# Kernel tuning notes

Measured on AMD Instinct MI355X. Metric: run time of the kernel, lower is better.

## Reference

```python
import jax, jax.numpy as jnp
import numpy as np


def lstm_dir(x, w_ih, w_hh, b, reverse):
    # x: [N, L, E]; torch gate order i, f, g, o; b = b_ih + b_hh combined
    if reverse:
        x = x[:, ::-1, :]
    H = w_hh.shape[1]
    N = x.shape[0]
    xg = jnp.einsum('nle,ge->nlg', x, w_ih) + b  # [N, L, 4H]
    def step(carry, xt):
        h, c = carry
        g = xt + h @ w_hh.T
        i, f, gg, o = jnp.split(g, 4, axis=-1)
        c = jax.nn.sigmoid(f) * c + jax.nn.sigmoid(i) * jnp.tanh(gg)
        h = jax.nn.sigmoid(o) * jnp.tanh(c)
        return (h, c), h
    init = (jnp.zeros((N, H), x.dtype), jnp.zeros((N, H), x.dtype))
    _, hs = jax.lax.scan(step, init, jnp.swapaxes(xg, 0, 1))
    hs = jnp.swapaxes(hs, 0, 1)  # [N, L, H]
    if reverse:
        hs = hs[:, ::-1, :]
    return hs


def setup_inputs() -> dict:
    key = jax.random.key(0)
    ks = jax.random.split(key, 10)
    B, D, S, V, E, H = 32, 32, 64, 32000, 256, 512
    tok = jax.random.randint(ks[0], (B, D, S), 1, V)
    slen = jax.random.randint(ks[1], (B, D), 8, S + 1)  # ragged sentence lengths
    docs = jnp.where(jnp.arange(S)[None, None, :] < slen[..., None], tok, 0)
    doc_lens = jax.random.randint(ks[2], (B,), 1, D + 1)  # ragged doc lengths
    embed_weight = jax.random.normal(ks[3], (V, E), jnp.float32) * 0.02
    def p(k, shp):
        return jax.random.normal(k, shp, jnp.float32) * 0.05
    return dict(
        docs=docs, doc_lens=doc_lens, max_doc_len=D,
        embed_weight=embed_weight,
        w_ih_f=p(ks[4], (4 * H, E)), w_hh_f=p(ks[5], (4 * H, H)), b_f=p(ks[6], (4 * H,)),
        w_ih_b=p(ks[7], (4 * H, E)), w_hh_b=p(ks[8], (4 * H, H)), b_b=p(ks[9], (4 * H,)),
    )


def reference(docs, doc_lens, max_doc_len, embed_weight, w_ih_f, w_hh_f, b_f, w_ih_b, w_hh_b, b_b):
    B, D, S = docs.shape
    sents = docs.reshape(B * D, S)                     # all sentences, incl. invalid slots
    sent_lens = jnp.sum(jnp.sign(sents), axis=1)       # nonzero-token count per sentence
    x = embed_weight[sents]                            # [BD, S, E]
    out_f = lstm_dir(x, w_ih_f, w_hh_f, b_f, False)
    out_b = lstm_dir(x, w_ih_b, w_hh_b, b_b, True)
    out = jnp.concatenate([out_f, out_b], axis=-1)     # [BD, S, 2H]
    # avg_pool1d over first sent_lens timesteps (segment mean)
    tmask = (jnp.arange(S)[None, :] < sent_lens[:, None]).astype(out.dtype)
    denom = jnp.maximum(sent_lens, 1).astype(out.dtype)
    pooled = jnp.sum(out * tmask[:, :, None], axis=1) / denom[:, None]  # [BD, 2H]
    pooled = pooled.reshape(B, D, -1)
    # pad_doc: zero out sentence slots beyond each doc_len (scatter-pad)
    dmask = jnp.arange(D)[None, :] < doc_lens[:, None]
    return jnp.where(dmask[:, :, None], pooled, jnp.zeros((), pooled.dtype))
```

## Files before the change

kernel.cpp:

```cpp
#include <hip/hip_runtime.h>
#include <hip/hip_bf16.h>
#include <hip/hip_cooperative_groups.h>

namespace cg = cooperative_groups;

typedef __attribute__((ext_vector_type(4))) float f32x4;
typedef __attribute__((ext_vector_type(8))) short s16x8;

#define SEQ   64
#define EMB   256
#define HID   512
#define NROW  1024
#define NTHR  512
#define NGRID 256
#define LDS_BYTES 98304

#define XB_OFF   0ull
#define WHH_OFF  (XB_OFF + 65536ull * EMB * 2)
#define WIH_OFF  (WHH_OFF + 2ull * 2048 * HID * 2)
#define HB_OFF   (WIH_OFF + 2ull * 2048 * EMB * 2)
#define SL_OFF   (HB_OFF + 4ull * NROW * HID * 2)
#define BAR_OFF  (SL_OFF + 4096ull)
#define XCDW_OFF (BAR_OFF + 64ull)

__device__ __forceinline__ unsigned short f2bf(float f) {
    union { float f; unsigned u; } x; x.f = f;
    unsigned r = x.u + 0x7fffu + ((x.u >> 16) & 1u);
    return (unsigned short)(r >> 16);
}
__device__ __forceinline__ void cvt8(unsigned short* dst, const float* src) {
    f32x4 v0 = *(const f32x4*)src;
    f32x4 v1 = *(const f32x4*)(src + 4);
    s16x8 o;
    o[0] = (short)f2bf(v0[0]); o[1] = (short)f2bf(v0[1]);
    o[2] = (short)f2bf(v0[2]); o[3] = (short)f2bf(v0[3]);
    o[4] = (short)f2bf(v1[0]); o[5] = (short)f2bf(v1[1]);
    o[6] = (short)f2bf(v1[2]); o[7] = (short)f2bf(v1[3]);
    *(s16x8*)dst = o;
}
__device__ __forceinline__ float sigf(float x)  { return 1.0f / (1.0f + __expf(-x)); }
__device__ __forceinline__ float tanh_(float x) { return 2.0f / (1.0f + __expf(-2.0f * x)) - 1.0f; }

__global__ void __launch_bounds__(NTHR, 2)
lstm_enc(const int* __restrict__ docs, const int* __restrict__ doc_lens,
         const float* __restrict__ embed,
         const float* __restrict__ w_ih_f, const float* __restrict__ w_hh_f, const float* __restrict__ b_f,
         const float* __restrict__ w_ih_b, const float* __restrict__ w_hh_b, const float* __restrict__ b_b,
         float* __restrict__ out, unsigned char* __restrict__ ws)
{
    extern __shared__ unsigned short Wf[];

    unsigned short* xb  = (unsigned short*)(ws + XB_OFF);
    unsigned short* whh = (unsigned short*)(ws + WHH_OFF);
    unsigned short* wih = (unsigned short*)(ws + WIH_OFF);
    unsigned short* hb  = (unsigned short*)(ws + HB_OFF);
    int*       sl   = (int*)(ws + SL_OFF);
    unsigned*  bar  = (unsigned*)(ws + BAR_OFF);
    unsigned*  xcdw = (unsigned*)(ws + XCDW_OFF);

    const int tid = threadIdx.x;
    const int bid = blockIdx.x;
    const int gid = bid * NTHR + tid;

    for (int i = 0; i < 16; ++i) {
        int slot = gid + i * (NGRID * NTHR);
        int row = slot >> 5;
        int e   = (slot & 31) << 3;
        int tok = docs[row];
        cvt8(xb + (size_t)slot * 8, embed + (size_t)tok * EMB + e);
    }
    cvt8(whh + (size_t)gid * 8,             w_hh_f + (size_t)gid * 8);
    cvt8(whh + (size_t)(gid + 131072) * 8,  w_hh_b + (size_t)gid * 8);
    {
        int dir0 = gid >> 16;
        int idx  = gid & 65535;
        cvt8(wih + (size_t)gid * 8, (dir0 ? w_ih_b : w_ih_f) + (size_t)idx * 8);
    }
    {
        s16x8 z = {0,0,0,0,0,0,0,0};
        *(s16x8*)(hb + (size_t)gid * 8) = z;
    }
    if (gid < NROW) {
        int c = 0;
        const int* dr = docs + gid * SEQ;
        for (int s2 = 0; s2 < SEQ; ++s2) c += (dr[s2] != 0);
        sl[gid] = c;
    }
    if (gid < 8) bar[gid] = 0u;

    if (tid == 0) {
        unsigned xcd_id;
        asm("s_getreg_b32 %0, hwreg(HW_REG_XCC_ID)" : "=s"(xcd_id));
        __hip_atomic_store(xcdw + bid, xcd_id, __ATOMIC_RELAXED, __HIP_MEMORY_SCOPE_AGENT);
    }

    cg::this_grid().sync();

    const int grp = bid & 7;
    const int dir = grp >> 2;
    const int rg  = grp & 3;
    const int cgd = bid >> 3;
    const int rowbase = rg * 256;
    const int hubase  = cgd * 16;

    bool fast;
    {
        unsigned mine = __hip_atomic_load(xcdw + bid, __ATOMIC_RELAXED, __HIP_MEMORY_SCOPE_AGENT);
        unsigned same = 1u;
        for (int j = 0; j < 32; ++j) {
            unsigned o = __hip_atomic_load(xcdw + (grp + 8 * j), __ATOMIC_RELAXED, __HIP_MEMORY_SCOPE_AGENT);
            same &= (o == mine) ? 1u : 0u;
        }
        fast = (same != 0u);
    }

    {
        const unsigned short* whh_d = whh + (size_t)dir * 2048 * HID;
        const unsigned short* wih_d = wih + (size_t)dir * 2048 * EMB;
        for (int s2 = 0; s2 < 12; ++s2) {
            int S = s2 * NTHR + tid;
            int f = S >> 6, lane_s = S & 63;
            int kc = f >> 2, g = f & 3;
            int l15s = lane_s & 15, lqs = lane_s >> 4;
            int gn = g * HID + hubase + l15s;
            int k  = kc * 32 + lqs * 8;
            const unsigned short* src = (k < HID)
                ? (whh_d + (size_t)gn * HID + k)
                : (wih_d + (size_t)gn * EMB + (k - HID));
            *(s16x8*)(Wf + (size_t)S * 8) = *(const s16x8*)src;
        }
    }
    __syncthreads();

    const int wid = tid >> 6, lane = tid & 63, l15 = lane & 15, lq = lane >> 4;
    const int hu = hubase + l15;
    const float* bsrc = dir ? b_b : b_f;
    const float bi_ = bsrc[hu], bf_ = bsrc[HID + hu], bg_ = bsrc[2 * HID + hu], bo_ = bsrc[3 * HID + hu];

    int rA[2];
    rA[0] = rowbase + wid * 32 + l15;
    rA[1] = rowbase + wid * 32 + 16 + l15;

    int gr8[8]; int sl8[8]; float c8[8], pool8[8];
    #pragma unroll
    for (int rf = 0; rf < 2; ++rf)
        #pragma unroll
        for (int r = 0; r < 4; ++r) {
            int k8 = rf * 4 + r;
            gr8[k8] = rowbase + wid * 32 + rf * 16 + lq * 4 + r;
            sl8[k8] = sl[gr8[k8]];
            c8[k8] = 0.f; pool8[k8] = 0.f;
        }

    #pragma unroll 1
    for (int t = 0; t < SEQ; ++t) {
        const int te = dir ? (SEQ - 1 - t) : t;
        const unsigned short* hrd = hb + (size_t)((t & 1) * 2 + dir) * NROW * HID;
        unsigned short* hwr       = hb + (size_t)((((t + 1) & 1)) * 2 + dir) * NROW * HID;

        f32x4 acc[2][4];
        #pragma unroll
        for (int rf = 0; rf < 2; ++rf)
            #pragma unroll
            for (int g = 0; g < 4; ++g)
                acc[rf][g] = (f32x4){0.f, 0.f, 0.f, 0.f};

        auto ldA = [&](s16x8* dst, int kc) {
            #pragma unroll
            for (int rf = 0; rf < 2; ++rf) {
                const unsigned short* p = (kc < 16)
                    ? hrd + (size_t)rA[rf] * HID + kc * 32 + lq * 8
                    : xb + ((size_t)rA[rf] * SEQ + te) * EMB + (kc - 16) * 32 + lq * 8;
                dst[rf] = *(const s16x8*)p;
            }
        };

        s16x8 Abuf[2][2];
        ldA(Abuf[0], 0);
        #pragma unroll
        for (int kc = 0; kc < 24; ++kc) {
            if (kc < 23) ldA(Abuf[(kc + 1) & 1], kc + 1);
            s16x8 Bf[4];
            #pragma unroll
            for (int g = 0; g < 4; ++g)
                Bf[g] = *(const s16x8*)(Wf + ((size_t)(kc * 4 + g) * 64 + lane) * 8);
            #pragma unroll
            for (int rf = 0; rf < 2; ++rf)
                #pragma unroll
                for (int g = 0; g < 4; ++g)
                    acc[rf][g] = __builtin_amdgcn_mfma_f32_16x16x32_bf16(
                        Abuf[kc & 1][rf], Bf[g], acc[rf][g], 0, 0, 0);
        }

        unsigned short hv8[8];
        #pragma unroll
        for (int rf = 0; rf < 2; ++rf) {
            #pragma unroll
            for (int r = 0; r < 4; ++r) {
                int k8 = rf * 4 + r;
                float iv = acc[rf][0][r] + bi_;
                float fv = acc[rf][1][r] + bf_;
                float gv = acc[rf][2][r] + bg_;
                float ov = acc[rf][3][r] + bo_;
                float cc = sigf(fv) * c8[k8] + sigf(iv) * tanh_(gv);
                c8[k8] = cc;
                float hh = sigf(ov) * tanh_(cc);
                hv8[k8] = f2bf(hh);
                if (te < sl8[k8]) pool8[k8] += hh;
            }
        }
        if (fast) {
            #pragma unroll
            for (int k8 = 0; k8 < 8; ++k8)
                hwr[(size_t)gr8[k8] * HID + hu] = hv8[k8];
        } else {
            #pragma unroll
            for (int k8 = 0; k8 < 8; ++k8)
                __hip_atomic_store(hwr + (size_t)gr8[k8] * HID + hu, hv8[k8],
                                   __ATOMIC_RELAXED, __HIP_MEMORY_SCOPE_AGENT);
        }

        __syncthreads();
        if (tid == 0) {
            __hip_atomic_fetch_add(bar + grp, 1u, __ATOMIC_RELAXED, __HIP_MEMORY_SCOPE_AGENT);
            unsigned tgt = 32u * (unsigned)(t + 1);
            while (__hip_atomic_load(bar + grp, __ATOMIC_RELAXED, __HIP_MEMORY_SCOPE_AGENT) < tgt)
                __builtin_amdgcn_s_sleep(1);
            if (fast) {
                asm volatile("buffer_inv" ::: "memory");
            } else {
                (void)__hip_atomic_load(bar + grp, __ATOMIC_ACQUIRE, __HIP_MEMORY_SCOPE_AGENT);
            }
        }
        __syncthreads();
    }

    #pragma unroll
    for (int k8 = 0; k8 < 8; ++k8) {
        int gr = gr8[k8];
        int b = gr >> 5, d = gr & 31;
        float denom = (float)(sl8[k8] > 0 ? sl8[k8] : 1);
        float v = (d < doc_lens[b]) ? (pool8[k8] / denom) : 0.f;
        out[(size_t)gr * 1024 + (size_t)dir * HID + hu] = v;
    }
}

extern "C" void kernel_launch(void* const* d_in, const int* in_sizes, int n_in,
                              void* d_out, int out_size, void* d_ws, size_t ws_size,
                              hipStream_t stream) {
    const int*   docs     = (const int*)d_in[0];
    const int*   doc_lens = (const int*)d_in[1];
    const float* embed    = (const float*)d_in[3];
    const float* w_ih_f   = (const float*)d_in[4];
    const float* w_hh_f   = (const float*)d_in[5];
    const float* b_f      = (const float*)d_in[6];
    const float* w_ih_b   = (const float*)d_in[7];
    const float* w_hh_b   = (const float*)d_in[8];
    const float* b_b      = (const float*)d_in[9];
    float* out = (float*)d_out;
    unsigned char* wsp = (unsigned char*)d_ws;

    (void)in_sizes; (void)n_in; (void)out_size; (void)ws_size;

    hipFuncSetAttribute((const void*)lstm_enc,
                        hipFuncAttributeMaxDynamicSharedMemorySize, LDS_BYTES);

    void* args[] = { &docs, &doc_lens, &embed, &w_ih_f, &w_hh_f, &b_f,
                     &w_ih_b, &w_hh_b, &b_b, &out, &wsp };
    hipLaunchCooperativeKernel((void*)lstm_enc, dim3(NGRID), dim3(NTHR),
                               args, (unsigned)LDS_BYTES, stream);
}
```

Before: 1.090 ms.

## Overlap next-step input projection with barrier wait and pad barrier counters

Splits the per-step GEMM into an input-projection part (x·W_ih plus bias folded into the accumulator init) and a recurrent part (h·W_hh). After writing h, each block signals arrival and then computes the next timestep's input projection before waiting on the barrier, so that work hides the barrier latency. Barrier counters are also padded to separate cache lines per group to avoid false sharing. The accumulators now stay live across the barrier, which raises register pressure, and the fetch-add stays relaxed before the spin, relying on the existing release and acquire handling.

After: 1.013 ms. -7.1%, faster.

```diff
diff --git a/kernel.cpp b/kernel.cpp
--- a/kernel.cpp
+++ b/kernel.cpp
@@ -14,6 +14,7 @@
 #define NTHR  512
 #define NGRID 256
 #define LDS_BYTES 98304
+#define BSTRIDE 32
 
 #define XB_OFF   0ull
 #define WHH_OFF  (XB_OFF + 65536ull * EMB * 2)
@@ -21,7 +22,7 @@
 #define HB_OFF   (WIH_OFF + 2ull * 2048 * EMB * 2)
 #define SL_OFF   (HB_OFF + 4ull * NROW * HID * 2)
 #define BAR_OFF  (SL_OFF + 4096ull)
-#define XCDW_OFF (BAR_OFF + 64ull)
+#define XCDW_OFF (BAR_OFF + 8ull * BSTRIDE * 4ull)
 
 __device__ __forceinline__ unsigned short f2bf(float f) {
     union { float f; unsigned u; } x; x.f = f;
@@ -86,7 +87,7 @@
         for (int s2 = 0; s2 < SEQ; ++s2) c += (dr[s2] != 0);
         sl[gid] = c;
     }
-    if (gid < 8) bar[gid] = 0u;
+    if (gid < 8 * BSTRIDE) bar[gid] = 0u;
 
     if (tid == 0) {
         unsigned xcd_id;
@@ -102,6 +103,7 @@
     const int cgd = bid >> 3;
     const int rowbase = rg * 256;
     const int hubase  = cgd * 16;
+    unsigned* mybar = bar + grp * BSTRIDE;
 
     bool fast;
     {
@@ -135,7 +137,9 @@
     const int wid = tid >> 6, lane = tid & 63, l15 = lane & 15, lq = lane >> 4;
     const int hu = hubase + l15;
     const float* bsrc = dir ? b_b : b_f;
-    const float bi_ = bsrc[hu], bf_ = bsrc[HID + hu], bg_ = bsrc[2 * HID + hu], bo_ = bsrc[3 * HID + hu];
+    float bg4[4];
+    #pragma unroll
+    for (int g = 0; g < 4; ++g) bg4[g] = bsrc[g * HID + hu];
 
     int rA[2];
     rA[0] = rowbase + wid * 32 + l15;
@@ -152,44 +156,81 @@
             c8[k8] = 0.f; pool8[k8] = 0.f;
         }
 
+    f32x4 acc[2][4];
+
+    auto ldB = [&](s16x8* dst, int kc) {
+        #pragma unroll
+        for (int g = 0; g < 4; ++g)
+            dst[g] = *(const s16x8*)(Wf + ((size_t)(kc * 4 + g) * 64 + lane) * 8);
+    };
+    auto ldX = [&](s16x8* dst, int kc, int te2) {
+        #pragma unroll
+        for (int rf = 0; rf < 2; ++rf)
+            dst[rf] = *(const s16x8*)(xb + ((size_t)rA[rf] * SEQ + te2) * EMB + (kc - 16) * 32 + lq * 8);
+    };
+    auto ldH = [&](s16x8* dst, int kc, const unsigned short* hsrc) {
+        #pragma unroll
+        for (int rf = 0; rf < 2; ++rf)
+            dst[rf] = *(const s16x8*)(hsrc + (size_t)rA[rf] * HID + kc * 32 + lq * 8);
+    };
+    auto xpart = [&](int te2) {
+        #pragma unroll
+        for (int rf = 0; rf < 2; ++rf)
+            #pragma unroll
+            for (int g = 0; g < 4; ++g)
+                acc[rf][g] = (f32x4){bg4[g], bg4[g], bg4[g], bg4[g]};
+        s16x8 Ax[3][2];
+        ldX(Ax[0], 16, te2);
+        ldX(Ax[1], 17, te2);
+        #pragma unroll
+        for (int i = 0; i < 8; ++i) {
+            if (i + 2 < 8) ldX(Ax[(i + 2) % 3], 18 + i, te2);
+            s16x8 Bf[4]; ldB(Bf, 16 + i);
+            #pragma unroll
+            for (int rf = 0; rf < 2; ++rf)
+                #pragma unroll
+                for (int g = 0; g < 4; ++g)
+                    acc[rf][g] = __builtin_amdgcn_mfma_f32_16x16x32_bf16(
+                        Ax[i % 3][rf], Bf[g], acc[rf][g], 0, 0, 0);
+        }
+    };
+
+    xpart(dir ? (SEQ - 1) : 0);
+
     #pragma unroll 1
     for (int t = 0; t < SEQ; ++t) {
         const int te = dir ? (SEQ - 1 - t) : t;
         const unsigned short* hrd = hb + (size_t)((t & 1) * 2 + dir) * NROW * HID;
         unsigned short* hwr       = hb + (size_t)((((t + 1) & 1)) * 2 + dir) * NROW * HID;
 
-        f32x4 acc[2][4];
-        #pragma unroll
-        for (int rf = 0; rf < 2; ++rf)
-            #pragma unroll
-            for (int g = 0; g < 4; ++g)
-                acc[rf][g] = (f32x4){0.f, 0.f, 0.f, 0.f};
-
-        auto ldA = [&](s16x8* dst, int kc) {
-            #pragma unroll
-            for (int rf = 0; rf < 2; ++rf) {
-                const unsigned short* p = (kc < 16)
-                    ? hrd + (size_t)rA[rf] * HID + kc * 32 + lq * 8
-                    : xb + ((size_t)rA[rf] * SEQ + te) * EMB + (kc - 16) * 32 + lq * 8;
-                dst[rf] = *(const s16x8*)p;
+        __syncthreads();
+        if (tid == 0) {
+            unsigned tgt = 32u * (unsigned)t;
+            while (__hip_atomic_load(mybar, __ATOMIC_RELAXED, __HIP_MEMORY_SCOPE_AGENT) < tgt)
+                __builtin_amdgcn_s_sleep(1);
+            if (fast) {
+                asm volatile("buffer_inv" ::: "memory");
+            } else {
+                (void)__hip_atomic_load(mybar, __ATOMIC_ACQUIRE, __HIP_MEMORY_SCOPE_AGENT);
             }
-        };
-
-        s16x8 Abuf[2][2];
-        ldA(Abuf[0], 0);
-        #pragma unroll
-        for (int kc = 0; kc < 24; ++kc) {
-            if (kc < 23) ldA(Abuf[(kc + 1) & 1], kc + 1);
-            s16x8 Bf[4];
-            #pragma unroll
-            for (int g = 0; g < 4; ++g)
-                Bf[g] = *(const s16x8*)(Wf + ((size_t)(kc * 4 + g) * 64 + lane) * 8);
-            #pragma unroll
-            for (int rf = 0; rf < 2; ++rf)
+        }
+        __syncthreads();
+
+        {
+            s16x8 Ah[3][2];
+            ldH(Ah[0], 0, hrd);
+            ldH(Ah[1], 1, hrd);
+            #pragma unroll
+            for (int i = 0; i < 16; ++i) {
+                if (i + 2 < 16) ldH(Ah[(i + 2) % 3], i + 2, hrd);
+                s16x8 Bf[4]; ldB(Bf, i);
                 #pragma unroll
-                for (int g = 0; g < 4; ++g)
-                    acc[rf][g] = __builtin_amdgcn_mfma_f32_16x16x32_bf16(
-                        Abuf[kc & 1][rf], Bf[g], acc[rf][g], 0, 0, 0);
+                for (int rf = 0; rf < 2; ++rf)
+                    #pragma unroll
+                    for (int g = 0; g < 4; ++g)
+                        acc[rf][g] = __builtin_amdgcn_mfma_f32_16x16x32_bf16(
+                            Ah[i % 3][rf], Bf[g], acc[rf][g], 0, 0, 0);
+            }
         }
 
         unsigned short hv8[8];
@@ -198,10 +239,10 @@
             #pragma unroll
             for (int r = 0; r < 4; ++r) {
                 int k8 = rf * 4 + r;
-                float iv = acc[rf][0][r] + bi_;
-                float fv = acc[rf][1][r] + bf_;
-                float gv = acc[rf][2][r] + bg_;
-                float ov = acc[rf][3][r] + bo_;
+                float iv = acc[rf][0][r];
+                float fv = acc[rf][1][r];
+                float gv = acc[rf][2][r];
+                float ov = acc[rf][3][r];
                 float cc = sigf(fv) * c8[k8] + sigf(iv) * tanh_(gv);
                 c8[k8] = cc;
                 float hh = sigf(ov) * tanh_(cc);
@@ -221,18 +262,11 @@
         }
 
         __syncthreads();
-        if (tid == 0) {
-            __hip_atomic_fetch_add(bar + grp, 1u, __ATOMIC_RELAXED, __HIP_MEMORY_SCOPE_AGENT);
-            unsigned tgt = 32u * (unsigned)(t + 1);
-            while (__hip_atomic_load(bar + grp, __ATOMIC_RELAXED, __HIP_MEMORY_SCOPE_AGENT) < tgt)
-                __builtin_amdgcn_s_sleep(1);
-            if (fast) {
-                asm volatile("buffer_inv" ::: "memory");
-            } else {
-                (void)__hip_atomic_load(bar + grp, __ATOMIC_ACQUIRE, __HIP_MEMORY_SCOPE_AGENT);
-            }
-        }
-        __syncthreads();
+        if (t < SEQ - 1) {
+            if (tid == 0)
+                __hip_atomic_fetch_add(mybar, 1u, __ATOMIC_RELAXED, __HIP_MEMORY_SCOPE_AGENT);
+            xpart(dir ? (SEQ - 2 - t) : (t + 1));
+        }
     }
 
     #pragma unroll
```
